# Performance work log

Measured on AMD Instinct MI355X. Metric: run time of the kernel, lower is better.

## Reference

```python
import jax, jax.numpy as jnp
import numpy as np

B, S, H = 4, 2048, 1024
NH, NKV, HD = 16, 4, 64
EPS = 1e-6
SCALE = 1.0 / np.sqrt(HD)
N_REP = NH // NKV


def setup_inputs() -> dict:
    key = jax.random.key(0)
    ks = jax.random.split(key, 8)
    hidden_states = jax.random.normal(ks[0], (B, S, H), dtype=jnp.float32)
    # additive causal mask [1,1,S,S]: 0 on/below diagonal, -1e9 above
    causal_mask = jnp.where(
        jnp.tril(jnp.ones((S, S), dtype=bool)), 0.0, -1e9
    ).astype(jnp.float32)[None, None]
    # interleaved RoPE tables [S, HD] (each frequency repeated twice, matching _rotate_half's even/odd split)
    inv_freq = 1.0 / (10000.0 ** (np.arange(0, HD, 2, dtype=np.float32) / HD))
    angles = jnp.arange(S, dtype=jnp.float32)[:, None] * jnp.asarray(inv_freq)[None, :]
    emb = jnp.repeat(angles, 2, axis=-1)  # [S, HD]
    cos, sin = jnp.cos(emb), jnp.sin(emb)
    # learned params (stored [in, out] for einsum)
    Wq = jax.random.normal(ks[1], (H, NH * HD), dtype=jnp.float32) * 0.02
    Wk = jax.random.normal(ks[2], (H, NKV * HD), dtype=jnp.float32) * 0.02
    Wv = jax.random.normal(ks[3], (H, NKV * HD), dtype=jnp.float32) * 0.02
    Wo = jax.random.normal(ks[4], (NH * HD, H), dtype=jnp.float32) * 0.02
    q_norm_w = jnp.ones((HD,), dtype=jnp.float32)
    k_norm_w = jnp.ones((HD,), dtype=jnp.float32)
    return {"hidden_states": hidden_states, "causal_mask": causal_mask, "cos": cos,
            "sin": sin, "Wq": Wq, "Wk": Wk, "Wv": Wv, "Wo": Wo,
            "q_norm_w": q_norm_w, "k_norm_w": k_norm_w}


def _rms_norm(x, w):
    var = jnp.mean(jnp.square(x), axis=-1, keepdims=True)
    return x * jax.lax.rsqrt(var + EPS) * w


def _rotate_half(x):
    x1 = x[..., ::2]
    x2 = x[..., 1::2]
    return jnp.stack((-x2, x1), axis=-1).reshape(x.shape)


def reference(hidden_states, causal_mask, cos, sin, Wq, Wk, Wv, Wo, q_norm_w, k_norm_w):
    b, s, _ = hidden_states.shape
    q = jnp.einsum('bsh,hd->bsd', hidden_states, Wq).reshape(b, s, NH, HD)
    k = jnp.einsum('bsh,hd->bsd', hidden_states, Wk).reshape(b, s, NKV, HD)
    v = jnp.einsum('bsh,hd->bsd', hidden_states, Wv).reshape(b, s, NKV, HD)
    q = _rms_norm(q, q_norm_w)
    k = _rms_norm(k, k_norm_w)
    q = q.transpose(0, 2, 1, 3)  # [b, NH, s, HD]
    k = k.transpose(0, 2, 1, 3)  # [b, NKV, s, HD]
    v = v.transpose(0, 2, 1, 3)
    c = cos[None, None]  # [1,1,s,HD]
    sn = sin[None, None]
    q = q * c + _rotate_half(q) * sn
    k = k * c + _rotate_half(k) * sn
    if N_REP > 1:
        k = jnp.repeat(k, N_REP, axis=1)  # GQA expand -> [b, NH, s, HD]
        v = jnp.repeat(v, N_REP, axis=1)
    scores = jnp.einsum('bhqd,bhkd->bhqk', q, k) * SCALE + causal_mask
    probs = jax.nn.softmax(scores, axis=-1)
    attn = jnp.einsum('bhqk,bhkd->bhqd', probs, v)
    attn = attn.transpose(0, 2, 1, 3).reshape(b, s, NH * HD)
    return jnp.einsum('bsd,dh->bsh', attn, Wo)
```

## Files before the change

kernel.cpp:

```cpp
#include <hip/hip_runtime.h>

typedef unsigned short u16;
typedef unsigned int u32;

typedef __attribute__((ext_vector_type(8))) short bf16x8;
typedef __attribute__((ext_vector_type(4))) float f32x4;

#define QSCALE 0.18033688011112042f

__device__ __forceinline__ u16 f2bf(float x) {
    union { float f; u32 u; } v; v.f = x;
    u32 r = (v.u + 0x7FFFu + ((v.u >> 16) & 1u)) >> 16;
    return (u16)r;
}
__device__ __forceinline__ float bf2f(u16 x) {
    union { u32 u; float f; } v; v.u = ((u32)x) << 16;
    return v.f;
}
__device__ __forceinline__ u32 pk2(float x, float y) {
    u32 ax = __float_as_uint(x) + 0x8000u;
    u32 ay = __float_as_uint(y) + 0x8000u;
    return __builtin_amdgcn_perm(ay, ax, 0x07060302u);
}

__device__ __forceinline__ void cp16(const u16* g, u16* l) {
    __builtin_amdgcn_global_load_lds(
        (__attribute__((address_space(1))) void*)(g),
        (__attribute__((address_space(3))) void*)(l), 16, 0, 0);
}

__global__ void k_prep(const float* __restrict__ hidden, u16* __restrict__ hA,
                       const float* __restrict__ Wq, u16* __restrict__ WqT,
                       const float* __restrict__ Wk, u16* __restrict__ WkT,
                       const float* __restrict__ Wv, u16* __restrict__ WvT,
                       const float* __restrict__ Wo, u16* __restrict__ WoT) {
    __shared__ u16 t[64][72];
    int bid = blockIdx.x, tid = threadIdx.x;
    if (bid < 4096) {
        int i = (bid * 256 + tid) * 8;
        float4 a = *(const float4*)(hidden + i);
        float4 b = *(const float4*)(hidden + i + 4);
        ushort4 o0; o0.x = f2bf(a.x); o0.y = f2bf(a.y); o0.z = f2bf(a.z); o0.w = f2bf(a.w);
        ushort4 o1; o1.x = f2bf(b.x); o1.y = f2bf(b.y); o1.z = f2bf(b.z); o1.w = f2bf(b.w);
        *(ushort4*)(hA + i) = o0;
        *(ushort4*)(hA + i + 4) = o1;
        return;
    }
    int rb = bid - 4096;
    const float* W; u16* Wt; int N, bx, by;
    if (rb < 256)      { W = Wq; Wt = WqT; N = 1024; bx = rb & 15; by = rb >> 4; }
    else if (rb < 320) { W = Wk; Wt = WkT; N = 256;  rb -= 256; bx = rb & 3; by = rb >> 2; }
    else if (rb < 384) { W = Wv; Wt = WvT; N = 256;  rb -= 320; bx = rb & 3; by = rb >> 2; }
    else               { W = Wo; Wt = WoT; N = 1024; rb -= 384; bx = rb & 15; by = rb >> 4; }
    const int K = 1024;
    int rr = tid >> 2;
    int cs = tid & 3;
    const float* src = W + (by*64 + rr)*N + bx*64 + cs*16;
#pragma unroll
    for (int j = 0; j < 16; j += 4) {
        float4 v = *(const float4*)(src + j);
        t[rr][cs*16 + j + 0] = f2bf(v.x);
        t[rr][cs*16 + j + 1] = f2bf(v.y);
        t[rr][cs*16 + j + 2] = f2bf(v.z);
        t[rr][cs*16 + j + 3] = f2bf(v.w);
    }
    __syncthreads();
    u16* dst = Wt + (bx*64 + rr)*K + by*64 + cs*16;
#pragma unroll
    for (int j = 0; j < 16; ++j) dst[j] = t[cs*16 + j][rr];
}

__device__ __forceinline__ void stage_ab(const u16* __restrict__ Asrc, const u16* __restrict__ Bsrc,
                                         int kt, u16* At, u16* Bt, int tid, int wv) {
#pragma unroll
    for (int i = 0; i < 2; ++i) {
        int q = i*256 + tid;
        int r = q >> 2, sidx = q & 3;
        int s = sidx ^ ((r >> 1) & 3);
        cp16(Asrc + r*1024 + kt*32 + s*8, At + (i*256 + wv*64)*8);
        cp16(Bsrc + r*1024 + kt*32 + s*8, Bt + (i*256 + wv*64)*8);
    }
}

__global__ __launch_bounds__(256) void k_gemm(
    const u16* __restrict__ A,
    const u16* __restrict__ Bq, const u16* __restrict__ Bk, const u16* __restrict__ Bv,
    float* __restrict__ outF,
    u16* __restrict__ outQ, u16* __restrict__ outK, u16* __restrict__ outV,
    int mode)
{
    __shared__ __align__(16) u16 At[2][128*32];
    __shared__ __align__(16) u16 Bt[2][128*32];
    int tid = threadIdx.x;
    int lane = tid & 63, wv = tid >> 6;
    int l15 = lane & 15, quad = lane >> 4;
    int wm = wv >> 1, wn = wv & 1;
    int mb = blockIdx.x, nb = blockIdx.y;

    const u16* Bsrc; int target; int colLocal0;
    if (mode == 0)      { Bsrc = Bq + nb*128*1024;      target = 3; colLocal0 = nb*128; }
    else if (nb < 8)    { Bsrc = Bq + nb*128*1024;      target = 0; colLocal0 = nb*128; }
    else if (nb < 10)   { Bsrc = Bk + (nb-8)*128*1024;  target = 1; colLocal0 = (nb-8)*128; }
    else                { Bsrc = Bv + (nb-10)*128*1024; target = 2; colLocal0 = (nb-10)*128; }
    const u16* Asrc = A + mb*128*1024;

    f32x4 zf = {0.f, 0.f, 0.f, 0.f};
    f32x4 acc[4][4];
#pragma unroll
    for (int i = 0; i < 4; ++i)
#pragma unroll
        for (int j = 0; j < 4; ++j) acc[i][j] = zf;

    stage_ab(Asrc, Bsrc, 0, At[0], Bt[0], tid, wv);
    __syncthreads();

    for (int kt = 0; kt < 32; ++kt) {
        int cur = kt & 1;
        if (kt < 31) stage_ab(Asrc, Bsrc, kt + 1, At[cur ^ 1], Bt[cur ^ 1], tid, wv);
        bf16x8 af[4], bfr[4];
#pragma unroll
        for (int mt = 0; mt < 4; ++mt) {
            int row = wm*64 + mt*16 + l15;
            int sidx = quad ^ ((row >> 1) & 3);
            af[mt] = *(const bf16x8*)(At[cur] + row*32 + sidx*8);
        }
#pragma unroll
        for (int nt = 0; nt < 4; ++nt) {
            int row = wn*64 + nt*16 + l15;
            int sidx = quad ^ ((row >> 1) & 3);
            bfr[nt] = *(const bf16x8*)(Bt[cur] + row*32 + sidx*8);
        }
#pragma unroll
        for (int mt = 0; mt < 4; ++mt)
#pragma unroll
            for (int nt = 0; nt < 4; ++nt)
                acc[mt][nt] = __builtin_amdgcn_mfma_f32_16x16x32_bf16(bfr[nt], af[mt], acc[mt][nt], 0, 0, 0);
        __syncthreads();
    }

#pragma unroll
    for (int mt = 0; mt < 4; ++mt) {
        int row = mb*128 + wm*64 + mt*16 + l15;
#pragma unroll
        for (int nt = 0; nt < 4; ++nt) {
            int cb = colLocal0 + wn*64 + nt*16 + quad*4;
            f32x4 v = acc[mt][nt];
            if (target == 3) {
                *(f32x4*)(outF + row*1024 + cb) = v;
            } else {
                int b = row >> 11, s = row & 2047;
                int hh = cb >> 6, d = cb & 63;
                uint2 w; w.x = pk2(v[0], v[1]); w.y = pk2(v[2], v[3]);
                if (target == 0)      *(uint2*)(outQ + ((b*16 + hh)*2048 + s)*64 + d) = w;
                else if (target == 1) *(uint2*)(outK + ((b*4  + hh)*2048 + s)*64 + d) = w;
                else                  *(uint2*)(outV + ((b*4  + hh)*2048 + s)*64 + d) = w;
            }
        }
    }
}

__global__ void k_nv(u16* __restrict__ Q, u16* __restrict__ K,
                     const float* __restrict__ qw, const float* __restrict__ kw,
                     const float* __restrict__ cosp, const float* __restrict__ sinp,
                     const u16* __restrict__ V, u16* __restrict__ VT)
{
    __shared__ u16 t[64][72];
    int bid = blockIdx.x, tid = threadIdx.x;
    if (bid < 20480) {
        int row = bid * 8 + (tid >> 5);
        int tl = tid & 31;
        u16* base; const float* w; int s; float post;
        if (row < 131072) { base = Q + row*64; s = row & 2047; w = qw; post = QSCALE; }
        else { int r2 = row - 131072; base = K + r2*64; s = r2 & 2047; w = kw; post = 1.0f; }
        u32 packed = *(const u32*)(base + 2*tl);
        float x0 = bf2f((u16)(packed & 0xffffu));
        float x1 = bf2f((u16)(packed >> 16));
        float ss = x0*x0 + x1*x1;
#pragma unroll
        for (int m = 1; m < 32; m <<= 1) ss += __shfl_xor(ss, m, 32);
        float inv = rsqrtf(ss * (1.0f/64.0f) + 1e-6f);
        float w0 = w[2*tl], w1 = w[2*tl+1];
        float c = cosp[s*64 + 2*tl], sn = sinp[s*64 + 2*tl];
        float xn0 = x0 * inv * w0, xn1 = x1 * inv * w1;
        float y0 = (xn0*c - xn1*sn) * post;
        float y1 = (xn1*c + xn0*sn) * post;
        *(u32*)(base + 2*tl) = pk2(y0, y1);
        return;
    }
    int idx = bid - 20480;
    int sb = idx & 31, bh = idx >> 5;
    int r = tid >> 2, cs = tid & 3;
    const u16* src = V + (bh*2048 + sb*64 + r)*64 + cs*16;
    uint4 v0 = *(const uint4*)(src);
    uint4 v1 = *(const uint4*)(src + 8);
    *(uint4*)&t[r][cs*16]     = v0;
    *(uint4*)&t[r][cs*16 + 8] = v1;
    __syncthreads();
    u16* dst = VT + (bh*64 + r)*2048 + sb*64 + cs*16;
#pragma unroll
    for (int j = 0; j < 16; ++j) dst[j] = t[cs*16 + j][r];
}

__device__ __forceinline__ void stage_kv(const u16* __restrict__ Kg, const u16* __restrict__ Vg,
                                         int kt, u16* sK, u16* sV, int tid, int wv) {
#pragma unroll
    for (int i = 0; i < 2; ++i) {
        int q = i*256 + tid;
        int r = q >> 3, sidx = q & 7;
        int s = sidx ^ (r & 7);
        cp16(Kg + (kt*64 + r)*64 + s*8, sK + (i*256 + wv*64)*8);
        cp16(Vg + r*2048 + kt*64 + s*8, sV + (i*256 + wv*64)*8);
    }
}

__global__ __launch_bounds__(256, 4) void k_attn(
    const u16* __restrict__ Q, const u16* __restrict__ K,
    const u16* __restrict__ VT, u16* __restrict__ attn)
{
    __shared__ __align__(16) u16 smemP[64*64];
    __shared__ __align__(16) u16 smemK[64*64];
    __shared__ __align__(16) u16 smemV[64*64];

    int tid = threadIdx.x;
    int lane = tid & 63, wv = tid >> 6;
    int l15 = lane & 15, quad = lane >> 4;
    int p = blockIdx.x;
    int h = blockIdx.y, b = blockIdx.z;
    const u16* Kg = K + ((b*4 + (h >> 2))*2048)*64;
    const u16* Vg = VT + (b*4 + (h >> 2))*64*2048;

    int qcol = wv*16 + l15;

#pragma unroll
    for (int t = 0; t < 2; ++t) {
        int qi = t ? p : (31 - p);
        int q0 = qi * 64;
        const u16* Qg = Q + ((b*16 + h)*2048 + q0)*64;

        bf16x8 qf[2];
#pragma unroll
        for (int ks = 0; ks < 2; ++ks)
            qf[ks] = *(const bf16x8*)(Qg + (wv*16 + l15)*64 + ks*32 + quad*8);

        f32x4 zf = {0.f, 0.f, 0.f, 0.f};
        f32x4 o[4];
#pragma unroll
        for (int mt = 0; mt < 4; ++mt) o[mt] = zf;
        float l_q = 0.f;
        int qrow = q0 + wv*16 + l15;

        for (int kt = 0; kt <= qi; ++kt) {
            stage_kv(Kg, Vg, kt, smemK, smemV, tid, wv);
            __syncthreads();

            f32x4 sc[4];
#pragma unroll
            for (int mt = 0; mt < 4; ++mt) sc[mt] = zf;
#pragma unroll
            for (int ks = 0; ks < 2; ++ks) {
                bf16x8 kf[4];
#pragma unroll
                for (int mt = 0; mt < 4; ++mt) {
                    int row = mt*16 + l15;
                    int sidx = (ks*4 + quad) ^ (row & 7);
                    kf[mt] = *(const bf16x8*)(smemK + row*64 + sidx*8);
                }
#pragma unroll
                for (int mt = 0; mt < 4; ++mt)
                    sc[mt] = __builtin_amdgcn_mfma_f32_16x16x32_bf16(kf[mt], qf[ks], sc[mt], 0, 0, 0);
            }

            if (kt == qi) {
                int keyb = kt*64 + quad*4;
#pragma unroll
                for (int mt = 0; mt < 4; ++mt)
#pragma unroll
                    for (int r = 0; r < 4; ++r)
                        if (keyb + mt*16 + r > qrow) sc[mt][r] = -1e30f;
            }
            float rs = 0.f;
#pragma unroll
            for (int mt = 0; mt < 4; ++mt) {
                float p0 = __builtin_amdgcn_exp2f(sc[mt][0]);
                float p1 = __builtin_amdgcn_exp2f(sc[mt][1]);
                float p2 = __builtin_amdgcn_exp2f(sc[mt][2]);
                float p3 = __builtin_amdgcn_exp2f(sc[mt][3]);
                rs += (p0 + p1) + (p2 + p3);
                uint2 w; w.x = pk2(p0, p1); w.y = pk2(p2, p3);
                int gw = (mt*2 + (quad >> 1)) ^ (qcol & 7);
                *(uint2*)(smemP + qcol*64 + gw*8 + (quad & 1)*4) = w;
            }
            l_q += rs;

#pragma unroll
            for (int ks2 = 0; ks2 < 2; ++ks2) {
                int gr = (ks2*4 + quad) ^ (qcol & 7);
                bf16x8 pf = *(const bf16x8*)(smemP + qcol*64 + gr*8);
                bf16x8 vf[4];
#pragma unroll
                for (int mt = 0; mt < 4; ++mt) {
                    int row = mt*16 + l15;
                    int sidx = (ks2*4 + quad) ^ (row & 7);
                    vf[mt] = *(const bf16x8*)(smemV + row*64 + sidx*8);
                }
#pragma unroll
                for (int mt = 0; mt < 4; ++mt)
                    o[mt] = __builtin_amdgcn_mfma_f32_16x16x32_bf16(vf[mt], pf, o[mt], 0, 0, 0);
            }
            __syncthreads();
        }

        float lt = l_q;
        lt += __shfl_xor(lt, 16);
        lt += __shfl_xor(lt, 32);
        float rl = 1.0f / lt;
#pragma unroll
        for (int mt = 0; mt < 4; ++mt) {
            uint2 w;
            w.x = pk2(o[mt][0]*rl, o[mt][1]*rl);
            w.y = pk2(o[mt][2]*rl, o[mt][3]*rl);
            int gw = (mt*2 + (quad >> 1)) ^ (qcol & 7);
            *(uint2*)(smemP + qcol*64 + gw*8 + (quad & 1)*4) = w;
        }
        __syncthreads();
        {
            int r2 = tid >> 2, c = tid & 3;
            u16* dst = attn + (b*2048 + q0 + r2)*1024 + h*64 + c*16;
            int g0 = (c*2) ^ (r2 & 7);
            int g1 = (c*2 + 1) ^ (r2 & 7);
            *(uint4*)(dst)     = *(const uint4*)(smemP + r2*64 + g0*8);
            *(uint4*)(dst + 8) = *(const uint4*)(smemP + r2*64 + g1*8);
        }
        __syncthreads();
    }
}

extern "C" void kernel_launch(void* const* d_in, const int* in_sizes, int n_in,
                              void* d_out, int out_size, void* d_ws, size_t ws_size,
                              hipStream_t stream) {
    const float* hidden = (const float*)d_in[0];
    const float* cosp = (const float*)d_in[2];
    const float* sinp = (const float*)d_in[3];
    const float* Wq = (const float*)d_in[4];
    const float* Wk = (const float*)d_in[5];
    const float* Wv = (const float*)d_in[6];
    const float* Wo = (const float*)d_in[7];
    const float* qw = (const float*)d_in[8];
    const float* kw = (const float*)d_in[9];
    float* out = (float*)d_out;

    char* ws = (char*)d_ws;
    u16* hA   = (u16*)(ws);
    u16* WqT  = (u16*)(ws + 16777216);
    u16* WkT  = (u16*)(ws + 18874368);
    u16* WvT  = (u16*)(ws + 19398656);
    u16* WoT  = (u16*)(ws + 19922944);
    u16* Qws  = (u16*)(ws + 22020096);
    u16* Kws  = (u16*)(ws + 38797312);
    u16* Vws  = (u16*)(ws + 42991616);
    u16* VTw  = (u16*)(ws + 47185920);
    u16* attn = hA;

    k_prep<<<4736, 256, 0, stream>>>(hidden, hA, Wq, WqT, Wk, WkT, Wv, WvT, Wo, WoT);
    k_gemm<<<dim3(64, 12), 256, 0, stream>>>(hA, WqT, WkT, WvT, nullptr, Qws, Kws, Vws, 1);
    k_nv<<<20992, 256, 0, stream>>>(Qws, Kws, qw, kw, cosp, sinp, Vws, VTw);
    k_attn<<<dim3(16, 16, 4), 256, 0, stream>>>(Qws, Kws, VTw, attn);
    k_gemm<<<dim3(64, 8), 256, 0, stream>>>(attn, WoT, nullptr, nullptr, out, nullptr, nullptr, nullptr, 0);
}
```

Measured before the change: 256.0 us.

## Fuse QK RMSNorm+RoPE into QKV GEMM epilogue and double-buffer attention K/V

Swaps MFMA operand order so each lane holds a column of the output tile, then applies RMSNorm, RoPE and the query scale directly in the QKV GEMM epilogue with lane shuffles. This removes the separate read-modify-write pass over Q and K, leaving a standalone V-transpose kernel. The attention kernel now double-buffers the K/V shared-memory tiles so the next tile's async copy overlaps with compute. In exchange, epilogue stores become scalar, less-coalesced writes, and attention shared-memory use grows.

```diff
diff --git a/kernel.cpp b/kernel.cpp
--- a/kernel.cpp
+++ b/kernel.cpp
@@ -87,6 +87,8 @@
     const u16* __restrict__ Bq, const u16* __restrict__ Bk, const u16* __restrict__ Bv,
     float* __restrict__ outF,
     u16* __restrict__ outQ, u16* __restrict__ outK, u16* __restrict__ outV,
+    const float* __restrict__ qw, const float* __restrict__ kw,
+    const float* __restrict__ cosp, const float* __restrict__ sinp,
     int mode)
 {
     __shared__ __align__(16) u16 At[2][128*32];
@@ -134,61 +136,71 @@
         for (int mt = 0; mt < 4; ++mt)
 #pragma unroll
             for (int nt = 0; nt < 4; ++nt)
-                acc[mt][nt] = __builtin_amdgcn_mfma_f32_16x16x32_bf16(bfr[nt], af[mt], acc[mt][nt], 0, 0, 0);
+                acc[mt][nt] = __builtin_amdgcn_mfma_f32_16x16x32_bf16(af[mt], bfr[nt], acc[mt][nt], 0, 0, 0);
         __syncthreads();
     }
 
-#pragma unroll
-    for (int mt = 0; mt < 4; ++mt) {
-        int row = mb*128 + wm*64 + mt*16 + l15;
-#pragma unroll
-        for (int nt = 0; nt < 4; ++nt) {
-            int cb = colLocal0 + wn*64 + nt*16 + quad*4;
-            f32x4 v = acc[mt][nt];
-            if (target == 3) {
-                *(f32x4*)(outF + row*1024 + cb) = v;
-            } else {
+    if (target == 3) {
+#pragma unroll
+        for (int mt = 0; mt < 4; ++mt)
+#pragma unroll
+            for (int nt = 0; nt < 4; ++nt)
+#pragma unroll
+                for (int rr = 0; rr < 4; ++rr) {
+                    int row = mb*128 + wm*64 + mt*16 + quad*4 + rr;
+                    int cl  = colLocal0 + wn*64 + nt*16 + l15;
+                    outF[row*1024 + cl] = acc[mt][nt][rr];
+                }
+    } else if (target == 2) {
+#pragma unroll
+        for (int mt = 0; mt < 4; ++mt)
+#pragma unroll
+            for (int nt = 0; nt < 4; ++nt)
+#pragma unroll
+                for (int rr = 0; rr < 4; ++rr) {
+                    int row = mb*128 + wm*64 + mt*16 + quad*4 + rr;
+                    int cl  = colLocal0 + wn*64 + nt*16 + l15;
+                    int b = row >> 11, s = row & 2047;
+                    int hh = cl >> 6, d = cl & 63;
+                    outV[((b*4 + hh)*2048 + s)*64 + d] = f2bf(acc[mt][nt][rr]);
+                }
+    } else {
+        const float* w = (target == 0) ? qw : kw;
+        float post = (target == 0) ? QSCALE : 1.0f;
+        int hh = (colLocal0 >> 6) + wn;
+        float sgn = (l15 & 1) ? 1.0f : -1.0f;
+#pragma unroll
+        for (int mt = 0; mt < 4; ++mt) {
+#pragma unroll
+            for (int rr = 0; rr < 4; ++rr) {
+                int row = mb*128 + wm*64 + mt*16 + quad*4 + rr;
                 int b = row >> 11, s = row & 2047;
-                int hh = cb >> 6, d = cb & 63;
-                uint2 w; w.x = pk2(v[0], v[1]); w.y = pk2(v[2], v[3]);
-                if (target == 0)      *(uint2*)(outQ + ((b*16 + hh)*2048 + s)*64 + d) = w;
-                else if (target == 1) *(uint2*)(outK + ((b*4  + hh)*2048 + s)*64 + d) = w;
-                else                  *(uint2*)(outV + ((b*4  + hh)*2048 + s)*64 + d) = w;
-            }
-        }
-    }
-}
-
-__global__ void k_nv(u16* __restrict__ Q, u16* __restrict__ K,
-                     const float* __restrict__ qw, const float* __restrict__ kw,
-                     const float* __restrict__ cosp, const float* __restrict__ sinp,
-                     const u16* __restrict__ V, u16* __restrict__ VT)
-{
+                float ss = 0.f;
+#pragma unroll
+                for (int nt = 0; nt < 4; ++nt) ss += acc[mt][nt][rr]*acc[mt][nt][rr];
+                ss += __shfl_xor(ss, 1); ss += __shfl_xor(ss, 2);
+                ss += __shfl_xor(ss, 4); ss += __shfl_xor(ss, 8);
+                float inv = rsqrtf(ss * (1.0f/64.0f) + 1e-6f);
+                u16* dstb = ((target == 0) ? outQ + ((b*16 + hh)*2048 + s)*64
+                                           : outK + ((b*4  + hh)*2048 + s)*64);
+#pragma unroll
+                for (int nt = 0; nt < 4; ++nt) {
+                    int d = nt*16 + l15;
+                    float x = acc[mt][nt][rr] * inv * w[d];
+                    float c = cosp[s*64 + d], sn = sinp[s*64 + d];
+                    float prt = __shfl_xor(x, 1);
+                    float y = (x*c + sgn*prt*sn) * post;
+                    dstb[d] = f2bf(y);
+                }
+            }
+        }
+    }
+}
+
+__global__ void k_vt(const u16* __restrict__ V, u16* __restrict__ VT) {
     __shared__ u16 t[64][72];
-    int bid = blockIdx.x, tid = threadIdx.x;
-    if (bid < 20480) {
-        int row = bid * 8 + (tid >> 5);
-        int tl = tid & 31;
-        u16* base; const float* w; int s; float post;
-        if (row < 131072) { base = Q + row*64; s = row & 2047; w = qw; post = QSCALE; }
-        else { int r2 = row - 131072; base = K + r2*64; s = r2 & 2047; w = kw; post = 1.0f; }
-        u32 packed = *(const u32*)(base + 2*tl);
-        float x0 = bf2f((u16)(packed & 0xffffu));
-        float x1 = bf2f((u16)(packed >> 16));
-        float ss = x0*x0 + x1*x1;
-#pragma unroll
-        for (int m = 1; m < 32; m <<= 1) ss += __shfl_xor(ss, m, 32);
-        float inv = rsqrtf(ss * (1.0f/64.0f) + 1e-6f);
-        float w0 = w[2*tl], w1 = w[2*tl+1];
-        float c = cosp[s*64 + 2*tl], sn = sinp[s*64 + 2*tl];
-        float xn0 = x0 * inv * w0, xn1 = x1 * inv * w1;
-        float y0 = (xn0*c - xn1*sn) * post;
-        float y1 = (xn1*c + xn0*sn) * post;
-        *(u32*)(base + 2*tl) = pk2(y0, y1);
-        return;
-    }
-    int idx = bid - 20480;
-    int sb = idx & 31, bh = idx >> 5;
+    int sb = blockIdx.x & 31, bh = blockIdx.x >> 5;
+    int tid = threadIdx.x;
     int r = tid >> 2, cs = tid & 3;
     const u16* src = V + (bh*2048 + sb*64 + r)*64 + cs*16;
     uint4 v0 = *(const uint4*)(src);
@@ -218,8 +230,8 @@
     const u16* __restrict__ VT, u16* __restrict__ attn)
 {
     __shared__ __align__(16) u16 smemP[64*64];
-    __shared__ __align__(16) u16 smemK[64*64];
-    __shared__ __align__(16) u16 smemV[64*64];
+    __shared__ __align__(16) u16 smemK[2][64*64];
+    __shared__ __align__(16) u16 smemV[2][64*64];
 
     int tid = threadIdx.x;
     int lane = tid & 63, wv = tid >> 6;
@@ -249,9 +261,12 @@
         float l_q = 0.f;
         int qrow = q0 + wv*16 + l15;
 
+        stage_kv(Kg, Vg, 0, smemK[0], smemV[0], tid, wv);
+        __syncthreads();
+
         for (int kt = 0; kt <= qi; ++kt) {
-            stage_kv(Kg, Vg, kt, smemK, smemV, tid, wv);
-            __syncthreads();
+            int cur = kt & 1;
+            if (kt < qi) stage_kv(Kg, Vg, kt + 1, smemK[cur ^ 1], smemV[cur ^ 1], tid, wv);
 
             f32x4 sc[4];
 #pragma unroll
@@ -263,7 +278,7 @@
                 for (int mt = 0; mt < 4; ++mt) {
                     int row = mt*16 + l15;
                     int sidx = (ks*4 + quad) ^ (row & 7);
-                    kf[mt] = *(const bf16x8*)(smemK + row*64 + sidx*8);
+                    kf[mt] = *(const bf16x8*)(smemK[cur] + row*64 + sidx*8);
                 }
 #pragma unroll
                 for (int mt = 0; mt < 4; ++mt)
@@ -301,7 +316,7 @@
                 for (int mt = 0; mt < 4; ++mt) {
                     int row = mt*16 + l15;
                     int sidx = (ks2*4 + quad) ^ (row & 7);
-                    vf[mt] = *(const bf16x8*)(smemV + row*64 + sidx*8);
+                    vf[mt] = *(const bf16x8*)(smemV[cur] + row*64 + sidx*8);
                 }
 #pragma unroll
                 for (int mt = 0; mt < 4; ++mt)
@@ -362,8 +377,11 @@
     u16* attn = hA;
 
     k_prep<<<4736, 256, 0, stream>>>(hidden, hA, Wq, WqT, Wk, WkT, Wv, WvT, Wo, WoT);
-    k_gemm<<<dim3(64, 12), 256, 0, stream>>>(hA, WqT, WkT, WvT, nullptr, Qws, Kws, Vws, 1);
-    k_nv<<<20992, 256, 0, stream>>>(Qws, Kws, qw, kw, cosp, sinp, Vws, VTw);
+    k_gemm<<<dim3(64, 12), 256, 0, stream>>>(hA, WqT, WkT, WvT, nullptr, Qws, Kws, Vws,
+                                             qw, kw, cosp, sinp, 1);
+    k_vt<<<512, 256, 0, stream>>>(Vws, VTw);
     k_attn<<<dim3(16, 16, 4), 256, 0, stream>>>(Qws, Kws, VTw, attn);
-    k_gemm<<<dim3(64, 8), 256, 0, stream>>>(attn, WoT, nullptr, nullptr, out, nullptr, nullptr, nullptr, 0);
-}
+    k_gemm<<<dim3(64, 8), 256, 0, stream>>>(attn, WoT, nullptr, nullptr, out,
+                                            nullptr, nullptr, nullptr,
+                                            nullptr, nullptr, nullptr, nullptr, 0);
+}
```

Result: no change. 255.4 us (-0.2%).
